# Performance work log

Measured on AMD Instinct MI355X. Metric: run time of the kernel, lower is better.

Reference implementation:

```python
import jax, jax.numpy as jnp
import numpy as np

MAX_REL = 11  # hardcoded max_relative_position in the module
BN_EPS = 1e-5


def _wn_linear(x, v, g):
    # torch weight_norm on Conv2d 1x1 (dim=0): w = g * v / ||v||_row
    w = v * (g / jnp.linalg.norm(v, axis=1))[:, None]
    return x @ w.T


def _rel_embed(table, lq, lk):
    dist = jnp.arange(lk)[None, :] - jnp.arange(lq)[:, None]
    idx = jnp.clip(dist, -MAX_REL, MAX_REL) + MAX_REL
    return table[idx]  # [lq, lk, d_k]


def setup_inputs() -> dict:
    key = jax.random.key(0)
    B, N, L, D, H = 32, 325, 12, 128, 8
    dk = D // H
    ks = jax.random.split(key, 12)
    rn = lambda k, s, sc=1.0: jax.random.normal(k, s, jnp.float32) * sc
    wq_v = rn(ks[0], (D, D), 1.0 / np.sqrt(D))
    wk_v = rn(ks[1], (D, D), 1.0 / np.sqrt(D))
    wv_v = rn(ks[2], (D, D), 1.0 / np.sqrt(D))
    fc_v = rn(ks[3], (D, D), 1.0 / np.sqrt(D))
    nrm = lambda v: jnp.linalg.norm(v, axis=1)  # weight_norm init: g = ||v||
    return {
        "input_Q": rn(ks[4], (B, N, L, D)),
        "input_K": rn(ks[5], (B, N, L, D)),
        "input_V": rn(ks[6], (B, N, L, D)),
        "wq_v": wq_v, "wq_g": nrm(wq_v),
        "wk_v": wk_v, "wk_g": nrm(wk_v),
        "wv_v": wv_v, "wv_g": nrm(wv_v),
        "fc_v": fc_v, "fc_g": nrm(fc_v),
        "rel_k": rn(ks[7], (2 * MAX_REL + 1, dk), np.sqrt(2.0 / (2 * MAX_REL + 1 + dk)) * np.sqrt(2.0)),
        "rel_v": rn(ks[8], (2 * MAX_REL + 1, dk), np.sqrt(2.0 / (2 * MAX_REL + 1 + dk)) * np.sqrt(2.0)),
        "w1": rn(ks[9], (H, H), np.sqrt(2.0 / H)),
        "w2": rn(ks[10], (H, H), np.sqrt(2.0 / H)),
        "bn_gamma": jnp.ones((D,), jnp.float32),
        "bn_beta": jnp.zeros((D,), jnp.float32),
    }


def reference(input_Q, input_K, input_V, wq_v, wq_g, wk_v, wk_g, wv_v, wv_g,
              fc_v, fc_g, rel_k, rel_v, w1, w2, bn_gamma, bn_beta):
    B, N, L, D = input_Q.shape
    H = w1.shape[0]
    dk = D // H
    scale = 1.0 / np.sqrt(dk)

    Q = _wn_linear(input_Q, wq_v, wq_g).reshape(B, N, L, H, dk)
    K = _wn_linear(input_K, wk_v, wk_g).reshape(B, N, L, H, dk)
    V = _wn_linear(input_V, wv_v, wv_g).reshape(B, N, L, H, dk)

    # content scores + relative-position key scores
    s1 = jnp.einsum('bnqhd,bnkhd->bnhqk', Q, K)
    K2 = _rel_embed(rel_k, L, L)                      # [L, L, dk]
    s2 = jnp.einsum('bnqhd,qkd->bnhqk', Q, K2)
    scores = (s1 + s2) * scale

    # learned cross-head mixing before softmax (w1)
    scores = jnp.einsum('bnhqk,hg->bngqk', scores, w1)
    attn = jax.nn.softmax(jax.nn.leaky_relu(scores, 0.2), axis=-1)
    # learned cross-head mixing after softmax (w2)
    attn = jnp.einsum('bnhqk,hg->bngqk', attn, w2)

    # dual context paths: V and relative-position V
    c1 = jnp.einsum('bnhqk,bnkhd->bnhqd', attn, V)
    V2 = _rel_embed(rel_v, L, L)                      # [L, L, dk]
    c2 = jnp.einsum('bnhqk,qkd->bnhqd', attn, V2)
    ctx = jnp.transpose(c1 + c2, (0, 1, 3, 2, 4)).reshape(B, N, L, D)

    # batch norm over (B, N, L) per channel (stand-in for RepresentativeBatchNorm2d)
    mean = ctx.mean(axis=(0, 1, 2))
    var = ctx.var(axis=(0, 1, 2))
    ctx_n = (ctx - mean) * jax.lax.rsqrt(var + BN_EPS) * bn_gamma + bn_beta

    out = _wn_linear(ctx_n, fc_v, fc_g)
    out = jax.nn.relu(out) + input_V

    attn_ret = jnp.transpose(attn, (3, 0, 1, 2, 4)).reshape(L, B * N * H, L)
    return out, attn_ret
```

## Files before the change

### kernel.cpp

```cpp
#include <hip/hip_runtime.h>
#include <math.h>

#define B_   32
#define N_   325
#define L_   12
#define D_   128
#define H_   8
#define DK_  16
#define BN_  (B_*N_)
#define ROWS_ (BN_*L_)
#define TAB_ 23
#define BNH_ (BN_*H_)
#define OUT_MAIN_ ((size_t)ROWS_ * D_)

#define XS_  136
#define QS_  132
#define RS_  17
#define KTS_ 13

typedef short v8s __attribute__((ext_vector_type(8)));
typedef float v4f __attribute__((ext_vector_type(4)));

__device__ __forceinline__ unsigned short f2bf_bits(float f) {
    unsigned int u = __float_as_uint(f);
    unsigned int r = (u + 0x7fffu + ((u >> 16) & 1u)) >> 16;
    return (unsigned short)r;
}

__global__ __launch_bounds__(64)
void prep_kernel(const float* __restrict__ wqv, const float* __restrict__ wqg,
                 const float* __restrict__ wkv, const float* __restrict__ wkg,
                 const float* __restrict__ wvv, const float* __restrict__ wvg,
                 const float* __restrict__ fcv, const float* __restrict__ fcg,
                 unsigned short* __restrict__ Wb, float* __restrict__ stats)
{
    const int b = blockIdx.x, t = threadIdx.x;
    if (b == 4*D_) {
        for (int j = t; j < 256; j += 64) stats[j] = 0.f;
        return;
    }
    const int m = b >> 7, o = b & 127;
    const float* v; const float* g;
    if      (m == 0) { v = wqv; g = wqg; }
    else if (m == 1) { v = wkv; g = wkg; }
    else if (m == 2) { v = wvv; g = wvg; }
    else             { v = fcv; g = fcg; }
    float x0 = v[o*D_ + t];
    float x1 = v[o*D_ + t + 64];
    float ss = x0*x0 + x1*x1;
    #pragma unroll
    for (int off = 32; off > 0; off >>= 1) ss += __shfl_down(ss, off, 64);
    ss = __shfl(ss, 0, 64);
    const float scale = g[o] / sqrtf(ss);
    unsigned short* W = Wb + m*(D_*D_);
    {
        int k = t;
        int off = ((o>>4)*4 + (k>>5))*512 + ((k>>3)&3)*128 + (o&15)*8 + (k&7);
        W[off] = f2bf_bits(x0*scale);
        k = t + 64;
        off = ((o>>4)*4 + (k>>5))*512 + ((k>>3)&3)*128 + (o&15)*8 + (k&7);
        W[off] = f2bf_bits(x1*scale);
    }
}

__global__ __launch_bounds__(192, 3)
void attn_kernel(const float* __restrict__ xq, const float* __restrict__ xk,
                 const float* __restrict__ xv,
                 const float* __restrict__ relk, const float* __restrict__ relv,
                 const float* __restrict__ w1g, const float* __restrict__ w2g,
                 const unsigned short* __restrict__ Wb,
                 float* __restrict__ outm, float* __restrict__ attn_out)
{
    __shared__ __align__(16) char smem[3*16*XS_*2];
    __shared__ __align__(16) float sQ[L_][QS_];
    __shared__ __align__(16) float sV[L_][QS_];
    __shared__ float sKt[H_*DK_*KTS_];
    __shared__ float sRk[TAB_*RS_];
    __shared__ float sRv[TAB_*RS_];
    __shared__ float sW1[H_*H_];
    __shared__ float sW2[H_*H_];

    unsigned short (*sXb)[16][XS_] =
        reinterpret_cast<unsigned short (*)[16][XS_]>(smem);
    float* pS  = (float*)smem;
    float* pS2 = pS + H_*L_*L_;

    const int tid = threadIdx.x;
    const int bn  = blockIdx.x;
    const size_t base = (size_t)bn * (L_*D_);

    #pragma unroll
    for (int mat = 0; mat < 3; ++mat) {
        const float* src = (mat == 0) ? xq : ((mat == 1) ? xk : xv);
        const float4* s4 = (const float4*)(src + base);
        for (int idx = tid; idx < L_*D_/4; idx += 192) {
            const int row = idx >> 5;
            const int c4  = (idx & 31) * 4;
            float4 v = s4[idx];
            ushort4 u;
            u.x = f2bf_bits(v.x); u.y = f2bf_bits(v.y);
            u.z = f2bf_bits(v.z); u.w = f2bf_bits(v.w);
            *(ushort4*)&sXb[mat][row][c4] = u;
        }
    }
    for (int idx = tid; idx < 3*272; idx += 192) {
        const int mat = idx / 272, o = idx - mat*272;
        ((unsigned int*)&sXb[mat][12][0])[o] = 0u;
    }
    for (int idx = tid; idx < TAB_*DK_; idx += 192) {
        const int r = idx >> 4, c = idx & 15;
        sRk[r*RS_ + c] = relk[idx];
        sRv[r*RS_ + c] = relv[idx];
    }
    if (tid < H_*H_) { sW1[tid] = w1g[tid]; sW2[tid] = w2g[tid]; }
    __syncthreads();

    {
        const int mat  = tid / 64;
        const int lane = tid & 63;
        const int quad = lane >> 4;
        const int c15  = lane & 15;
        v8s a[4];
        #pragma unroll
        for (int kk = 0; kk < 4; ++kk)
            a[kk] = *(const v8s*)&sXb[mat][c15][kk*32 + quad*8];
        const v8s* WB = (const v8s*)(Wb + mat*(D_*D_));
        const int token0 = quad*4;
        #pragma unroll
        for (int tile = 0; tile < 8; ++tile) {
            v4f acc = {0.f, 0.f, 0.f, 0.f};
            #pragma unroll
            for (int kk = 0; kk < 4; ++kk) {
                v8s bfrag = WB[(tile*4 + kk)*64 + lane];
                acc = __builtin_amdgcn_mfma_f32_16x16x32_bf16(a[kk], bfrag, acc, 0, 0, 0);
            }
            if (mat == 1) {
                #pragma unroll
                for (int r = 0; r < 4; ++r)
                    if (token0 + r < L_)
                        sKt[tile*(DK_*KTS_) + c15*KTS_ + token0 + r] = acc[r];
            } else {
                float (*dst)[QS_] = (mat == 0) ? sQ : sV;
                #pragma unroll
                for (int r = 0; r < 4; ++r)
                    if (token0 + r < L_)
                        dst[token0 + r][tile*16 + c15] = acc[r];
            }
        }
    }
    __syncthreads();

    for (int task = tid; task < H_*L_*L_; task += 192) {
        const int h = task / (L_*L_);
        const int r = task - h*(L_*L_);
        const int q = r / L_;
        const int k = r - q*L_;
        const float* Qp = &sQ[q][h*DK_];
        const float* Kp = &sKt[h*(DK_*KTS_) + k];
        const float* Rp = &sRk[(k - q + 11)*RS_];
        float s = 0.f;
        #pragma unroll
        for (int d = 0; d < DK_; ++d) s += Qp[d] * (Kp[d*KTS_] + Rp[d]);
        pS[task] = s * 0.25f;
    }
    __syncthreads();

    if (tid < H_*L_) {
        const int g = tid / L_;
        const int q = tid - g*L_;
        float vals[L_];
        float mx = -1e30f;
        #pragma unroll
        for (int k = 0; k < L_; ++k) {
            float a = 0.f;
            #pragma unroll
            for (int h = 0; h < H_; ++h) a += pS[h*(L_*L_) + q*L_ + k] * sW1[h*H_ + g];
            a = (a >= 0.f) ? a : 0.2f*a;
            vals[k] = a;
            mx = fmaxf(mx, a);
        }
        float sum = 0.f;
        #pragma unroll
        for (int k = 0; k < L_; ++k) { vals[k] = expf(vals[k] - mx); sum += vals[k]; }
        const float inv = 1.f / sum;
        #pragma unroll
        for (int k = 0; k < L_; ++k) pS2[g*(L_*L_) + q*L_ + k] = vals[k]*inv;
    }
    __syncthreads();

    for (int task = tid; task < H_*L_*L_; task += 192) {
        const int g = task / (L_*L_);
        const int r = task - g*(L_*L_);
        const int q = r / L_;
        const int k = r - q*L_;
        float a = 0.f;
        #pragma unroll
        for (int h = 0; h < H_; ++h) a += pS2[h*(L_*L_) + q*L_ + k] * sW2[h*H_ + g];
        pS[task] = a;
        attn_out[(size_t)q*((size_t)BNH_*L_) + ((size_t)bn*H_ + g)*L_ + k] = a;
    }
    __syncthreads();

    for (int task = tid; task < L_*D_; task += 192) {
        const int q = task >> 7;
        const int c = task & 127;
        const int h = c >> 4;
        const int d = c & 15;
        float a = 0.f;
        #pragma unroll
        for (int k = 0; k < L_; ++k)
            a += pS[h*(L_*L_) + q*L_ + k] * (sV[k][c] + sRv[(k - q + 11)*RS_ + d]);
        outm[((size_t)bn*L_ + q)*D_ + c] = a;
    }
}

__global__ __launch_bounds__(256)
void bnreduce_kernel(const float* __restrict__ outm, float* __restrict__ stats)
{
    const int tid  = threadIdx.x;
    const int c    = tid & 127;
    const int half = tid >> 7;
    float s = 0.f, s2 = 0.f;
    for (int r = blockIdx.x*2 + half; r < ROWS_; r += gridDim.x*2) {
        float v = outm[(size_t)r*D_ + c];
        s += v; s2 += v*v;
    }
    atomicAdd(&stats[c], s);
    atomicAdd(&stats[c+128], s2);
}

__global__ __launch_bounds__(128)
void bnfinal_kernel(const float* __restrict__ stats,
                    const float* __restrict__ gamma, const float* __restrict__ beta,
                    float* __restrict__ stats2)
{
    const int c = threadIdx.x;
    const float invn = 1.f / (float)ROWS_;
    float mean = stats[c]*invn;
    float var  = stats[c+128]*invn - mean*mean;
    float sc   = rsqrtf(var + 1e-5f) * gamma[c];
    stats2[c]     = sc;
    stats2[c+128] = beta[c] - mean*sc;
}

__global__ __launch_bounds__(256, 4)
void fc_kernel(float* __restrict__ outm, const float* __restrict__ stats2,
               const unsigned short* __restrict__ Wfc,
               const float* __restrict__ resid)
{
    __shared__ float sSS[256];
    __shared__ __align__(16) unsigned short sC[16][XS_];
    const int tid = threadIdx.x;
    const size_t row0 = (size_t)blockIdx.x * 16;

    sSS[tid] = stats2[tid];
    __syncthreads();
    for (int idx = tid; idx < 16*D_/4; idx += 256) {
        const int r  = idx >> 5;
        const int c4 = (idx & 31) * 4;
        float4 v = *(const float4*)&outm[(row0 + r)*D_ + c4];
        ushort4 u;
        u.x = f2bf_bits(v.x*sSS[c4+0] + sSS[128+c4+0]);
        u.y = f2bf_bits(v.y*sSS[c4+1] + sSS[128+c4+1]);
        u.z = f2bf_bits(v.z*sSS[c4+2] + sSS[128+c4+2]);
        u.w = f2bf_bits(v.w*sSS[c4+3] + sSS[128+c4+3]);
        *(ushort4*)&sC[r][c4] = u;
    }
    __syncthreads();

    const int wave = tid >> 6;
    const int lane = tid & 63;
    const int quad = lane >> 4;
    const int c15  = lane & 15;
    v8s a[4];
    #pragma unroll
    for (int kk = 0; kk < 4; ++kk)
        a[kk] = *(const v8s*)&sC[c15][kk*32 + quad*8];
    const v8s* WB = (const v8s*)Wfc;
    #pragma unroll
    for (int tt = 0; tt < 2; ++tt) {
        const int tile = wave*2 + tt;
        v4f acc = {0.f, 0.f, 0.f, 0.f};
        #pragma unroll
        for (int kk = 0; kk < 4; ++kk) {
            v8s bfrag = WB[(tile*4 + kk)*64 + lane];
            acc = __builtin_amdgcn_mfma_f32_16x16x32_bf16(a[kk], bfrag, acc, 0, 0, 0);
        }
        #pragma unroll
        for (int r = 0; r < 4; ++r) {
            const size_t aidx = (row0 + quad*4 + r)*D_ + tile*16 + c15;
            outm[aidx] = fmaxf(acc[r], 0.f) + resid[aidx];
        }
    }
}

extern "C" void kernel_launch(void* const* d_in, const int* in_sizes, int n_in,
                              void* d_out, int out_size, void* d_ws, size_t ws_size,
                              hipStream_t stream)
{
    const float* xq   = (const float*)d_in[0];
    const float* xk   = (const float*)d_in[1];
    const float* xv   = (const float*)d_in[2];
    const float* wqv  = (const float*)d_in[3];
    const float* wqg  = (const float*)d_in[4];
    const float* wkv  = (const float*)d_in[5];
    const float* wkg  = (const float*)d_in[6];
    const float* wvv  = (const float*)d_in[7];
    const float* wvg  = (const float*)d_in[8];
    const float* fcv  = (const float*)d_in[9];
    const float* fcg  = (const float*)d_in[10];
    const float* relk = (const float*)d_in[11];
    const float* relv = (const float*)d_in[12];
    const float* w1   = (const float*)d_in[13];
    const float* w2   = (const float*)d_in[14];
    const float* gam  = (const float*)d_in[15];
    const float* bet  = (const float*)d_in[16];

    unsigned short* Wb = (unsigned short*)d_ws;
    float* stats  = (float*)((char*)d_ws + 4*D_*D_*sizeof(unsigned short));
    float* stats2 = stats + 256;

    float* outm     = (float*)d_out;
    float* attn_out = outm + OUT_MAIN_;

    prep_kernel<<<4*D_ + 1, 64, 0, stream>>>(wqv,wqg, wkv,wkg, wvv,wvg, fcv,fcg,
                                             Wb, stats);
    attn_kernel<<<BN_, 192, 0, stream>>>(xq, xk, xv, relk, relv, w1, w2,
                                         Wb, outm, attn_out);
    bnreduce_kernel<<<512, 256, 0, stream>>>(outm, stats);
    bnfinal_kernel<<<1, 128, 0, stream>>>(stats, gam, bet, stats2);
    fc_kernel<<<ROWS_/16, 256, 0, stream>>>(outm, stats2, Wb + 3*D_*D_, xv);
}
```

Baseline: 488.5 us.

## Fuse batch-norm statistics into attention kernel and widen block to 256 threads

Removes the separate bnreduce kernel: the attention kernel now accumulates per-channel sum and sum-of-squares of its context output in shared memory and atomically adds them to global stats once per block. It also moves to 256 threads, spreading the 24 projection MFMA tiles across 4 waves, stores K row-major instead of transposed, and vectorises the score and context loops with float4 loads. This saves a full re-read of the context tensor but adds 256 global atomics per block (10400 blocks), plus shared atomics, which may contend.

```diff
diff --git a/kernel.cpp b/kernel.cpp
--- a/kernel.cpp
+++ b/kernel.cpp
@@ -14,9 +14,9 @@
 #define OUT_MAIN_ ((size_t)ROWS_ * D_)
 
 #define XS_  136
-#define QS_  132
-#define RS_  17
-#define KTS_ 13
+#define QS2_ 132
+#define RS2_ 20
+#define PSP_ 148
 
 typedef short v8s __attribute__((ext_vector_type(8)));
 typedef float v4f __attribute__((ext_vector_type(4)));
@@ -63,118 +63,124 @@
     }
 }
 
-__global__ __launch_bounds__(192, 3)
+__global__ __launch_bounds__(256, 4)
 void attn_kernel(const float* __restrict__ xq, const float* __restrict__ xk,
                  const float* __restrict__ xv,
                  const float* __restrict__ relk, const float* __restrict__ relv,
                  const float* __restrict__ w1g, const float* __restrict__ w2g,
                  const unsigned short* __restrict__ Wb,
-                 float* __restrict__ outm, float* __restrict__ attn_out)
+                 float* __restrict__ outm, float* __restrict__ attn_out,
+                 float* __restrict__ stats)
 {
     __shared__ __align__(16) char smem[3*16*XS_*2];
-    __shared__ __align__(16) float sQ[L_][QS_];
-    __shared__ __align__(16) float sV[L_][QS_];
-    __shared__ float sKt[H_*DK_*KTS_];
-    __shared__ float sRk[TAB_*RS_];
-    __shared__ float sRv[TAB_*RS_];
+    __shared__ __align__(16) float sQ[L_][QS2_];
+    __shared__ __align__(16) float sK[L_][QS2_];
+    __shared__ __align__(16) float sV[L_][QS2_];
+    __shared__ __align__(16) float sRk[TAB_*RS2_];
+    __shared__ __align__(16) float sRv[TAB_*RS2_];
     __shared__ float sW1[H_*H_];
     __shared__ float sW2[H_*H_];
+    __shared__ float sStats[256];
 
     unsigned short (*sXb)[16][XS_] =
         reinterpret_cast<unsigned short (*)[16][XS_]>(smem);
     float* pS  = (float*)smem;
-    float* pS2 = pS + H_*L_*L_;
+    float* pS2 = pS + 8*PSP_;
 
     const int tid = threadIdx.x;
     const int bn  = blockIdx.x;
     const size_t base = (size_t)bn * (L_*D_);
 
-    #pragma unroll
-    for (int mat = 0; mat < 3; ++mat) {
-        const float* src = (mat == 0) ? xq : ((mat == 1) ? xk : xv);
-        const float4* s4 = (const float4*)(src + base);
-        for (int idx = tid; idx < L_*D_/4; idx += 192) {
-            const int row = idx >> 5;
-            const int c4  = (idx & 31) * 4;
-            float4 v = s4[idx];
+    {
+        const float4* q4 = (const float4*)(xq + base);
+        const float4* k4 = (const float4*)(xk + base);
+        const float4* v4 = (const float4*)(xv + base);
+        for (int idx = tid; idx < 3*384; idx += 256) {
+            const int mat = idx / 384;
+            const int rem = idx - mat*384;
+            const int row = rem >> 5;
+            const int c4  = (rem & 31) * 4;
+            const float4* s4 = (mat == 0) ? q4 : ((mat == 1) ? k4 : v4);
+            float4 v = s4[rem];
             ushort4 u;
             u.x = f2bf_bits(v.x); u.y = f2bf_bits(v.y);
             u.z = f2bf_bits(v.z); u.w = f2bf_bits(v.w);
             *(ushort4*)&sXb[mat][row][c4] = u;
         }
-    }
-    for (int idx = tid; idx < 3*272; idx += 192) {
-        const int mat = idx / 272, o = idx - mat*272;
-        ((unsigned int*)&sXb[mat][12][0])[o] = 0u;
-    }
-    for (int idx = tid; idx < TAB_*DK_; idx += 192) {
-        const int r = idx >> 4, c = idx & 15;
-        sRk[r*RS_ + c] = relk[idx];
-        sRv[r*RS_ + c] = relv[idx];
-    }
-    if (tid < H_*H_) { sW1[tid] = w1g[tid]; sW2[tid] = w2g[tid]; }
+        for (int idx = tid; idx < TAB_*DK_; idx += 256) {
+            const int r = idx >> 4, c = idx & 15;
+            sRk[r*RS2_ + c] = relk[idx];
+            sRv[r*RS2_ + c] = relv[idx];
+        }
+        if (tid < H_*H_) { sW1[tid] = w1g[tid]; sW2[tid] = w2g[tid]; }
+        sStats[tid] = 0.f;
+    }
     __syncthreads();
 
     {
-        const int mat  = tid / 64;
+        const int wave = tid >> 6;
         const int lane = tid & 63;
         const int quad = lane >> 4;
         const int c15  = lane & 15;
-        v8s a[4];
-        #pragma unroll
-        for (int kk = 0; kk < 4; ++kk)
-            a[kk] = *(const v8s*)&sXb[mat][c15][kk*32 + quad*8];
-        const v8s* WB = (const v8s*)(Wb + mat*(D_*D_));
         const int token0 = quad*4;
         #pragma unroll
-        for (int tile = 0; tile < 8; ++tile) {
+        for (int i = 0; i < 6; ++i) {
+            const int cb   = wave*6 + i;
+            const int mat  = cb >> 3;
+            const int tile = cb & 7;
+            v8s a[4];
+            #pragma unroll
+            for (int kk = 0; kk < 4; ++kk)
+                a[kk] = *(const v8s*)&sXb[mat][c15][kk*32 + quad*8];
+            const v8s* WB = (const v8s*)(Wb + mat*(D_*D_));
             v4f acc = {0.f, 0.f, 0.f, 0.f};
             #pragma unroll
             for (int kk = 0; kk < 4; ++kk) {
                 v8s bfrag = WB[(tile*4 + kk)*64 + lane];
                 acc = __builtin_amdgcn_mfma_f32_16x16x32_bf16(a[kk], bfrag, acc, 0, 0, 0);
             }
-            if (mat == 1) {
-                #pragma unroll
-                for (int r = 0; r < 4; ++r)
-                    if (token0 + r < L_)
-                        sKt[tile*(DK_*KTS_) + c15*KTS_ + token0 + r] = acc[r];
-            } else {
-                float (*dst)[QS_] = (mat == 0) ? sQ : sV;
-                #pragma unroll
-                for (int r = 0; r < 4; ++r)
-                    if (token0 + r < L_)
-                        dst[token0 + r][tile*16 + c15] = acc[r];
-            }
-        }
-    }
-    __syncthreads();
-
-    for (int task = tid; task < H_*L_*L_; task += 192) {
-        const int h = task / (L_*L_);
-        const int r = task - h*(L_*L_);
-        const int q = r / L_;
-        const int k = r - q*L_;
+            float (*dst)[QS2_] = (mat == 0) ? sQ : ((mat == 1) ? sK : sV);
+            #pragma unroll
+            for (int r = 0; r < 4; ++r)
+                if (token0 + r < L_)
+                    dst[token0 + r][tile*16 + c15] = acc[r];
+        }
+    }
+    __syncthreads();
+
+    for (int task = tid; task < H_*L_*L_; task += 256) {
+        const int h = task / 144;
+        const int r = task - h*144;
+        const int q = r / 12;
+        const int k = r - q*12;
         const float* Qp = &sQ[q][h*DK_];
-        const float* Kp = &sKt[h*(DK_*KTS_) + k];
-        const float* Rp = &sRk[(k - q + 11)*RS_];
+        const float* Kp = &sK[k][h*DK_];
+        const float* Rp = &sRk[(k - q + 11)*RS2_];
         float s = 0.f;
         #pragma unroll
-        for (int d = 0; d < DK_; ++d) s += Qp[d] * (Kp[d*KTS_] + Rp[d]);
-        pS[task] = s * 0.25f;
+        for (int d4 = 0; d4 < 4; ++d4) {
+            v4f qv = *(const v4f*)(Qp + d4*4);
+            v4f kv = *(const v4f*)(Kp + d4*4);
+            v4f rv = *(const v4f*)(Rp + d4*4);
+            s += qv.x*(kv.x+rv.x);
+            s += qv.y*(kv.y+rv.y);
+            s += qv.z*(kv.z+rv.z);
+            s += qv.w*(kv.w+rv.w);
+        }
+        pS[h*PSP_ + r] = s * 0.25f;
     }
     __syncthreads();
 
     if (tid < H_*L_) {
-        const int g = tid / L_;
-        const int q = tid - g*L_;
+        const int g = tid / 12;
+        const int q = tid - g*12;
         float vals[L_];
         float mx = -1e30f;
         #pragma unroll
         for (int k = 0; k < L_; ++k) {
             float a = 0.f;
             #pragma unroll
-            for (int h = 0; h < H_; ++h) a += pS[h*(L_*L_) + q*L_ + k] * sW1[h*H_ + g];
+            for (int h = 0; h < H_; ++h) a += pS[h*PSP_ + q*12 + k] * sW1[h*H_ + g];
             a = (a >= 0.f) ? a : 0.2f*a;
             vals[k] = a;
             mx = fmaxf(mx, a);
@@ -184,49 +190,66 @@
         for (int k = 0; k < L_; ++k) { vals[k] = expf(vals[k] - mx); sum += vals[k]; }
         const float inv = 1.f / sum;
         #pragma unroll
-        for (int k = 0; k < L_; ++k) pS2[g*(L_*L_) + q*L_ + k] = vals[k]*inv;
-    }
-    __syncthreads();
-
-    for (int task = tid; task < H_*L_*L_; task += 192) {
-        const int g = task / (L_*L_);
-        const int r = task - g*(L_*L_);
-        const int q = r / L_;
-        const int k = r - q*L_;
+        for (int k = 0; k < L_; ++k) pS2[g*PSP_ + q*12 + k] = vals[k]*inv;
+    }
+    __syncthreads();
+
+    for (int task = tid; task < H_*L_*L_; task += 256) {
+        const int g = task / 144;
+        const int r = task - g*144;
+        const int q = r / 12;
+        const int k = r - q*12;
         float a = 0.f;
         #pragma unroll
-        for (int h = 0; h < H_; ++h) a += pS2[h*(L_*L_) + q*L_ + k] * sW2[h*H_ + g];
-        pS[task] = a;
+        for (int h = 0; h < H_; ++h) a += pS2[h*PSP_ + r] * sW2[h*H_ + g];
+        pS[g*PSP_ + r] = a;
         attn_out[(size_t)q*((size_t)BNH_*L_) + ((size_t)bn*H_ + g)*L_ + k] = a;
     }
     __syncthreads();
 
-    for (int task = tid; task < L_*D_; task += 192) {
-        const int q = task >> 7;
-        const int c = task & 127;
-        const int h = c >> 4;
-        const int d = c & 15;
-        float a = 0.f;
-        #pragma unroll
-        for (int k = 0; k < L_; ++k)
-            a += pS[h*(L_*L_) + q*L_ + k] * (sV[k][c] + sRv[(k - q + 11)*RS_ + d]);
-        outm[((size_t)bn*L_ + q)*D_ + c] = a;
-    }
-}
-
-__global__ __launch_bounds__(256)
-void bnreduce_kernel(const float* __restrict__ outm, float* __restrict__ stats)
-{
-    const int tid  = threadIdx.x;
-    const int c    = tid & 127;
-    const int half = tid >> 7;
-    float s = 0.f, s2 = 0.f;
-    for (int r = blockIdx.x*2 + half; r < ROWS_; r += gridDim.x*2) {
-        float v = outm[(size_t)r*D_ + c];
-        s += v; s2 += v*v;
-    }
-    atomicAdd(&stats[c], s);
-    atomicAdd(&stats[c+128], s2);
+    {
+        v4f s4  = {0.f, 0.f, 0.f, 0.f};
+        v4f s24 = {0.f, 0.f, 0.f, 0.f};
+        const int c4 = tid & 31;
+        const int c  = c4 * 4;
+        const int h  = c4 >> 2;
+        const int dd = c & 15;
+        for (int task = tid; task < L_*32; task += 256) {
+            const int q = task >> 5;
+            const float* Ap = &pS[h*PSP_ + q*12];
+            v4f a0 = *(const v4f*)(Ap);
+            v4f a1 = *(const v4f*)(Ap + 4);
+            v4f a2 = *(const v4f*)(Ap + 8);
+            const float av[12] = {a0.x,a0.y,a0.z,a0.w, a1.x,a1.y,a1.z,a1.w,
+                                  a2.x,a2.y,a2.z,a2.w};
+            v4f acc = {0.f, 0.f, 0.f, 0.f};
+            #pragma unroll
+            for (int k = 0; k < L_; ++k) {
+                const float a = av[k];
+                v4f vv = *(const v4f*)&sV[k][c];
+                v4f rv = *(const v4f*)&sRv[(k - q + 11)*RS2_ + dd];
+                acc.x += a*(vv.x+rv.x);
+                acc.y += a*(vv.y+rv.y);
+                acc.z += a*(vv.z+rv.z);
+                acc.w += a*(vv.w+rv.w);
+            }
+            *(v4f*)&outm[((size_t)bn*L_ + q)*D_ + c] = acc;
+            s4  += acc;
+            s24 += acc*acc;
+        }
+        const int lane = tid & 63;
+        #pragma unroll
+        for (int j = 0; j < 4; ++j) {
+            float a = s4[j]  + __shfl_down(s4[j],  32, 64);
+            float b = s24[j] + __shfl_down(s24[j], 32, 64);
+            if (lane < 32) {
+                atomicAdd(&sStats[c + j],       a);
+                atomicAdd(&sStats[128 + c + j], b);
+            }
+        }
+    }
+    __syncthreads();
+    atomicAdd(&stats[tid], sStats[tid]);
 }
 
 __global__ __launch_bounds__(128)
@@ -325,9 +348,8 @@
 
     prep_kernel<<<4*D_ + 1, 64, 0, stream>>>(wqv,wqg, wkv,wkg, wvv,wvg, fcv,fcg,
                                              Wb, stats);
-    attn_kernel<<<BN_, 192, 0, stream>>>(xq, xk, xv, relk, relv, w1, w2,
-                                         Wb, outm, attn_out);
-    bnreduce_kernel<<<512, 256, 0, stream>>>(outm, stats);
+    attn_kernel<<<BN_, 256, 0, stream>>>(xq, xk, xv, relk, relv, w1, w2,
+                                         Wb, outm, attn_out, stats);
     bnfinal_kernel<<<1, 128, 0, stream>>>(stats, gam, bet, stats2);
     fc_kernel<<<ROWS_/16, 256, 0, stream>>>(outm, stats2, Wb + 3*D_*D_, xv);
 }
```

Result: slower. 540.0 us (+10.5%).
